# Kernel optimization log

Measured on AMD Instinct MI355X. Metric: run time of the kernel, lower is better.

## Reference

```python
import jax, jax.numpy as jnp
import numpy as np

DUNITS = 1024
ATT_DIM = 1024
EPROJ = 1024
T = 16384
SCALING = 2.0


def setup_inputs() -> dict:
    key = jax.random.key(0)
    ks = jax.random.split(key, 8)
    dec_z = jax.random.normal(ks[0], (1, DUNITS), dtype=jnp.float32)
    att_prev = jnp.zeros((1, T), dtype=jnp.float32)
    pre_compute_enc_h = jax.random.normal(ks[1], (1, T, ATT_DIM), dtype=jnp.float32)
    enc_h = jax.random.normal(ks[2], (1, T, EPROJ), dtype=jnp.float32)
    mask = jnp.zeros((1, T), dtype=jnp.float32)
    # learned params: mlp_dec Linear(dunits->att_dim), gvec Linear(att_dim->1)
    W_dec = jax.random.normal(ks[3], (DUNITS, ATT_DIM), dtype=jnp.float32) / np.sqrt(DUNITS)
    b_dec = jnp.zeros((ATT_DIM,), dtype=jnp.float32)
    w_gvec = jax.random.normal(ks[4], (ATT_DIM,), dtype=jnp.float32) / np.sqrt(ATT_DIM)
    b_gvec = jnp.zeros((), dtype=jnp.float32)
    return {
        "dec_z": dec_z,
        "att_prev": att_prev,
        "pre_compute_enc_h": pre_compute_enc_h,
        "enc_h": enc_h,
        "mask": mask,
        "W_dec": W_dec,
        "b_dec": b_dec,
        "w_gvec": w_gvec,
        "b_gvec": b_gvec,
    }


def reference(dec_z, att_prev, pre_compute_enc_h, enc_h, mask, W_dec, b_dec, w_gvec, b_gvec):
    # dec_z: [1, dunits] -> mlp_dec -> [1, 1, att_dim]
    dec_z_tiled = (dec_z @ W_dec + b_dec)[:, None, :]
    # gvec(tanh(pre + tile)).squeeze(2): [1, T]
    e = jnp.einsum("bta,a->bt", jnp.tanh(pre_compute_enc_h + dec_z_tiled), w_gvec) + b_gvec
    e = e + mask
    w = jax.nn.softmax(SCALING * e, axis=1)  # [1, T]
    c = jnp.einsum("bte,bt->be", enc_h, w)   # [1, eproj]
    return (c, w)
```

## Files before the change

### kernel.cpp

```cpp
#include <hip/hip_runtime.h>
#include <math.h>

#define TT   16384
#define ADIM 1024
#define NCH  512
#define RPW  8
#define NCH2 64

__device__ __forceinline__ float ftanh(float x) {
    float e2 = __expf(2.0f * x);
    return 1.0f - 2.0f * __builtin_amdgcn_rcpf(e2 + 1.0f);
}

__global__ void k1_gemv_part(const float* __restrict__ z, const float* __restrict__ W,
                             float* __restrict__ part) {
    int b = blockIdx.x, tid = threadIdx.x;
    float4 acc = {0.f, 0.f, 0.f, 0.f};
#pragma unroll
    for (int i = 0; i < 4; ++i) {
        int d = b * 4 + i;
        float zv = z[d];
        float4 w4 = reinterpret_cast<const float4*>(W)[(size_t)d * 256 + tid];
        acc.x += zv * w4.x; acc.y += zv * w4.y; acc.z += zv * w4.z; acc.w += zv * w4.w;
    }
    reinterpret_cast<float4*>(part)[(size_t)b * 256 + tid] = acc;
}

__global__ void k2_gemv_red(const float* __restrict__ part, const float* __restrict__ bdec,
                            float* __restrict__ dp) {
    int b = blockIdx.x, tid = threadIdx.x;
    int lane = tid & 63, wv = tid >> 6;
    int rsub = lane >> 2;
    int colg = lane & 3;
    float4 acc = {0.f, 0.f, 0.f, 0.f};
#pragma unroll
    for (int i = 0; i < 4; ++i) {
        int row = i * 64 + wv * 16 + rsub;
        float4 v = reinterpret_cast<const float4*>(part)[(size_t)row * 256 + b * 4 + colg];
        acc.x += v.x; acc.y += v.y; acc.z += v.z; acc.w += v.w;
    }
#pragma unroll
    for (int off = 4; off <= 32; off <<= 1) {
        acc.x += __shfl_xor(acc.x, off, 64);
        acc.y += __shfl_xor(acc.y, off, 64);
        acc.z += __shfl_xor(acc.z, off, 64);
        acc.w += __shfl_xor(acc.w, off, 64);
    }
    __shared__ float4 lds[4][4];
    if (lane < 4) lds[wv][lane] = acc;
    __syncthreads();
    if (tid < 4) {
        float4 t = {0.f, 0.f, 0.f, 0.f};
#pragma unroll
        for (int w = 0; w < 4; ++w) {
            float4 v = lds[w][tid];
            t.x += v.x; t.y += v.y; t.z += v.z; t.w += v.w;
        }
        float4 bd = reinterpret_cast<const float4*>(bdec)[b * 4 + tid];
        t.x += bd.x; t.y += bd.y; t.z += bd.z; t.w += bd.w;
        reinterpret_cast<float4*>(dp)[b * 4 + tid] = t;
    }
}

__global__ void __launch_bounds__(256) k3_fused(
    const float* __restrict__ pre, const float* __restrict__ enc,
    const float* __restrict__ dp, const float* __restrict__ wg,
    const float* __restrict__ bgp, const float* __restrict__ mask,
    float* __restrict__ e_out, float* __restrict__ m_out,
    float* __restrict__ s_out, float* __restrict__ cpart) {
    int b = blockIdx.x, tid = threadIdx.x;
    int lane = tid & 63, wv = tid >> 6;
    float4 d4[4], g4[4];
    const float4* dp4 = reinterpret_cast<const float4*>(dp);
    const float4* wg4 = reinterpret_cast<const float4*>(wg);
#pragma unroll
    for (int j = 0; j < 4; ++j) { d4[j] = dp4[j * 64 + lane]; g4[j] = wg4[j * 64 + lane]; }
    float bgv = bgp[0];
    float m = -3.0e38f, s = 0.f;
    float4 ca[4] = {{0,0,0,0},{0,0,0,0},{0,0,0,0},{0,0,0,0}};
    int t0 = b * (4 * RPW) + wv * RPW;
    for (int i = 0; i < RPW; ++i) {
        int t = t0 + i;
        const float4* pr = reinterpret_cast<const float4*>(pre) + (size_t)t * 256;
        const float4* er = reinterpret_cast<const float4*>(enc) + (size_t)t * 256;
        float4 p[4], ev[4];
#pragma unroll
        for (int j = 0; j < 4; ++j) { p[j] = pr[j * 64 + lane]; ev[j] = er[j * 64 + lane]; }
        float dot = 0.f;
#pragma unroll
        for (int j = 0; j < 4; ++j) {
            dot += ftanh(p[j].x + d4[j].x) * g4[j].x;
            dot += ftanh(p[j].y + d4[j].y) * g4[j].y;
            dot += ftanh(p[j].z + d4[j].z) * g4[j].z;
            dot += ftanh(p[j].w + d4[j].w) * g4[j].w;
        }
#pragma unroll
        for (int off = 32; off; off >>= 1) dot += __shfl_xor(dot, off, 64);
        float et = 2.0f * (dot + bgv + mask[t]);
        if (lane == 0) e_out[t] = et;
        float mn = fmaxf(m, et);
        float sc = __expf(m - mn);
        float pp = __expf(et - mn);
        s = s * sc + pp;
#pragma unroll
        for (int j = 0; j < 4; ++j) {
            ca[j].x = ca[j].x * sc + pp * ev[j].x;
            ca[j].y = ca[j].y * sc + pp * ev[j].y;
            ca[j].z = ca[j].z * sc + pp * ev[j].z;
            ca[j].w = ca[j].w * sc + pp * ev[j].w;
        }
        m = mn;
    }
    __shared__ float lm[4], ls[4];
    __shared__ float4 lc[4][256];
#pragma unroll
    for (int j = 0; j < 4; ++j) lc[wv][j * 64 + lane] = ca[j];
    if (lane == 0) { lm[wv] = m; ls[wv] = s; }
    __syncthreads();
    float Mb = fmaxf(fmaxf(lm[0], lm[1]), fmaxf(lm[2], lm[3]));
    float s0 = __expf(lm[0] - Mb), s1 = __expf(lm[1] - Mb);
    float s2 = __expf(lm[2] - Mb), s3 = __expf(lm[3] - Mb);
    if (tid == 0) {
        m_out[b] = Mb;
        s_out[b] = ls[0] * s0 + ls[1] * s1 + ls[2] * s2 + ls[3] * s3;
    }
    float4 v0 = lc[0][tid], v1 = lc[1][tid], v2 = lc[2][tid], v3 = lc[3][tid];
    float4 o;
    o.x = v0.x * s0 + v1.x * s1 + v2.x * s2 + v3.x * s3;
    o.y = v0.y * s0 + v1.y * s1 + v2.y * s2 + v3.y * s3;
    o.z = v0.z * s0 + v1.z * s1 + v2.z * s2 + v3.z * s3;
    o.w = v0.w * s0 + v1.w * s1 + v2.w * s2 + v3.w * s3;
    reinterpret_cast<float4*>(cpart)[(size_t)b * 256 + tid] = o;
}

__global__ void __launch_bounds__(256) k4_fold(
    const float* __restrict__ m_arr, const float* __restrict__ s_arr,
    const float* __restrict__ cpart, float* __restrict__ cpart2,
    float* __restrict__ msout) {
    int b = blockIdx.x, tid = threadIdx.x;
    int lane = tid & 63, wv = tid >> 6;
    __shared__ float redm[4], reds[4];
    float mloc = fmaxf(m_arr[tid], m_arr[tid + 256]);
#pragma unroll
    for (int off = 32; off; off >>= 1) mloc = fmaxf(mloc, __shfl_xor(mloc, off, 64));
    if (lane == 0) redm[wv] = mloc;
    __syncthreads();
    float M = fmaxf(fmaxf(redm[0], redm[1]), fmaxf(redm[2], redm[3]));
    float4 acc = {0.f, 0.f, 0.f, 0.f};
#pragma unroll
    for (int i = 0; i < 8; ++i) {
        int r = b * 8 + i;
        float sc = __expf(m_arr[r] - M);
        float4 v = reinterpret_cast<const float4*>(cpart)[(size_t)r * 256 + tid];
        acc.x += sc * v.x; acc.y += sc * v.y; acc.z += sc * v.z; acc.w += sc * v.w;
    }
    reinterpret_cast<float4*>(cpart2)[(size_t)b * 256 + tid] = acc;
    if (b == 0) {
        float sl = s_arr[tid] * __expf(m_arr[tid] - M)
                 + s_arr[tid + 256] * __expf(m_arr[tid + 256] - M);
#pragma unroll
        for (int off = 32; off; off >>= 1) sl += __shfl_xor(sl, off, 64);
        if (lane == 0) reds[wv] = sl;
        __syncthreads();
        if (tid == 0) {
            float S = reds[0] + reds[1] + reds[2] + reds[3];
            msout[0] = M;
            msout[1] = 1.0f / S;
        }
    }
}

__global__ void __launch_bounds__(256) k5_final(
    const float* __restrict__ cpart2, const float* __restrict__ e,
    const float* __restrict__ ms, float* __restrict__ c_out,
    float* __restrict__ w_out) {
    int b = blockIdx.x, tid = threadIdx.x;
    float M = ms[0], invS = ms[1];
    if (b < 16) {
        int rs = tid >> 4;
        int cg = tid & 15;
        float4 acc = {0.f, 0.f, 0.f, 0.f};
#pragma unroll
        for (int i = 0; i < 4; ++i) {
            int r = rs * 4 + i;
            float4 v = reinterpret_cast<const float4*>(cpart2)[(size_t)r * 256 + b * 16 + cg];
            acc.x += v.x; acc.y += v.y; acc.z += v.z; acc.w += v.w;
        }
        __shared__ float4 lds[16][16];
        lds[rs][cg] = acc;
        __syncthreads();
        if (tid < 16) {
            float4 t = {0.f, 0.f, 0.f, 0.f};
#pragma unroll
            for (int r = 0; r < 16; ++r) {
                float4 v = lds[r][tid];
                t.x += v.x; t.y += v.y; t.z += v.z; t.w += v.w;
            }
            t.x *= invS; t.y *= invS; t.z *= invS; t.w *= invS;
            reinterpret_cast<float4*>(c_out)[b * 16 + tid] = t;
        }
    } else {
        int base = (b - 16) * 256 + tid;
        float4 ev = reinterpret_cast<const float4*>(e)[base];
        float4 w;
        w.x = __expf(ev.x - M) * invS;
        w.y = __expf(ev.y - M) * invS;
        w.z = __expf(ev.z - M) * invS;
        w.w = __expf(ev.w - M) * invS;
        reinterpret_cast<float4*>(w_out)[base] = w;
    }
}

extern "C" void kernel_launch(void* const* d_in, const int* in_sizes, int n_in,
                              void* d_out, int out_size, void* d_ws, size_t ws_size,
                              hipStream_t stream) {
    const float* dec_z = (const float*)d_in[0];
    const float* pre   = (const float*)d_in[2];
    const float* enc   = (const float*)d_in[3];
    const float* mask  = (const float*)d_in[4];
    const float* W_dec = (const float*)d_in[5];
    const float* b_dec = (const float*)d_in[6];
    const float* wg    = (const float*)d_in[7];
    const float* bg    = (const float*)d_in[8];

    float* out   = (float*)d_out;
    float* c_out = out;
    float* w_out = out + ADIM;

    float* ws = (float*)d_ws;
    float* part   = ws;
    float* dp     = part + 256 * ADIM;
    float* e_sc   = dp + ADIM;
    float* m_arr  = e_sc + TT;
    float* s_arr  = m_arr + NCH;
    float* cpart  = s_arr + NCH;
    float* cpart2 = cpart + (size_t)NCH * ADIM;
    float* ms     = cpart2 + (size_t)NCH2 * ADIM;

    k1_gemv_part<<<256, 256, 0, stream>>>(dec_z, W_dec, part);
    k2_gemv_red<<<64, 256, 0, stream>>>(part, b_dec, dp);
    k3_fused<<<NCH, 256, 0, stream>>>(pre, enc, dp, wg, bg, mask,
                                      e_sc, m_arr, s_arr, cpart);
    k4_fold<<<NCH2, 256, 0, stream>>>(m_arr, s_arr, cpart, cpart2, ms);
    k5_final<<<32, 256, 0, stream>>>(cpart2, e_sc, ms, c_out, w_out);
}
```

Before: 38.01 us.

## Double chunk count and split score and context passes for memory-level parallelism

```diff
diff --git a/kernel.cpp b/kernel.cpp
--- a/kernel.cpp
+++ b/kernel.cpp
@@ -3,8 +3,8 @@
 
 #define TT   16384
 #define ADIM 1024
-#define NCH  512
-#define RPW  8
+#define NCH  1024
+#define RPW  4
 #define NCH2 64
 
 __device__ __forceinline__ float ftanh(float x) {
@@ -76,41 +76,53 @@
 #pragma unroll
     for (int j = 0; j < 4; ++j) { d4[j] = dp4[j * 64 + lane]; g4[j] = wg4[j * 64 + lane]; }
     float bgv = bgp[0];
-    float m = -3.0e38f, s = 0.f;
+    int t0 = b * (4 * RPW) + wv * RPW;
+
+    float et[RPW];
+#pragma unroll
+    for (int i = 0; i < RPW; ++i) {
+        const float4* pr = reinterpret_cast<const float4*>(pre) + (size_t)(t0 + i) * 256;
+        float dot = 0.f;
+#pragma unroll
+        for (int j = 0; j < 4; ++j) {
+            float4 p = pr[j * 64 + lane];
+            dot += ftanh(p.x + d4[j].x) * g4[j].x;
+            dot += ftanh(p.y + d4[j].y) * g4[j].y;
+            dot += ftanh(p.z + d4[j].z) * g4[j].z;
+            dot += ftanh(p.w + d4[j].w) * g4[j].w;
+        }
+        et[i] = dot;
+    }
+#pragma unroll
+    for (int i = 0; i < RPW; ++i) {
+#pragma unroll
+        for (int off = 32; off; off >>= 1) et[i] += __shfl_xor(et[i], off, 64);
+        et[i] = 2.0f * (et[i] + bgv + mask[t0 + i]);
+    }
+    if (lane == 0) {
+#pragma unroll
+        for (int i = 0; i < RPW; ++i) e_out[t0 + i] = et[i];
+    }
+
+    float m = et[0];
+#pragma unroll
+    for (int i = 1; i < RPW; ++i) m = fmaxf(m, et[i]);
+    float p[RPW], s = 0.f;
+#pragma unroll
+    for (int i = 0; i < RPW; ++i) { p[i] = __expf(et[i] - m); s += p[i]; }
+
     float4 ca[4] = {{0,0,0,0},{0,0,0,0},{0,0,0,0},{0,0,0,0}};
-    int t0 = b * (4 * RPW) + wv * RPW;
+#pragma unroll
     for (int i = 0; i < RPW; ++i) {
-        int t = t0 + i;
-        const float4* pr = reinterpret_cast<const float4*>(pre) + (size_t)t * 256;
-        const float4* er = reinterpret_cast<const float4*>(enc) + (size_t)t * 256;
-        float4 p[4], ev[4];
-#pragma unroll
-        for (int j = 0; j < 4; ++j) { p[j] = pr[j * 64 + lane]; ev[j] = er[j * 64 + lane]; }
-        float dot = 0.f;
+        const float4* er = reinterpret_cast<const float4*>(enc) + (size_t)(t0 + i) * 256;
 #pragma unroll
         for (int j = 0; j < 4; ++j) {
-            dot += ftanh(p[j].x + d4[j].x) * g4[j].x;
-            dot += ftanh(p[j].y + d4[j].y) * g4[j].y;
-            dot += ftanh(p[j].z + d4[j].z) * g4[j].z;
-            dot += ftanh(p[j].w + d4[j].w) * g4[j].w;
-        }
-#pragma unroll
-        for (int off = 32; off; off >>= 1) dot += __shfl_xor(dot, off, 64);
-        float et = 2.0f * (dot + bgv + mask[t]);
-        if (lane == 0) e_out[t] = et;
-        float mn = fmaxf(m, et);
-        float sc = __expf(m - mn);
-        float pp = __expf(et - mn);
-        s = s * sc + pp;
-#pragma unroll
-        for (int j = 0; j < 4; ++j) {
-            ca[j].x = ca[j].x * sc + pp * ev[j].x;
-            ca[j].y = ca[j].y * sc + pp * ev[j].y;
-            ca[j].z = ca[j].z * sc + pp * ev[j].z;
-            ca[j].w = ca[j].w * sc + pp * ev[j].w;
-        }
-        m = mn;
-    }
+            float4 v = er[j * 64 + lane];
+            ca[j].x += p[i] * v.x; ca[j].y += p[i] * v.y;
+            ca[j].z += p[i] * v.z; ca[j].w += p[i] * v.w;
+        }
+    }
+
     __shared__ float lm[4], ls[4];
     __shared__ float4 lc[4][256];
 #pragma unroll
@@ -140,7 +152,9 @@
     int b = blockIdx.x, tid = threadIdx.x;
     int lane = tid & 63, wv = tid >> 6;
     __shared__ float redm[4], reds[4];
-    float mloc = fmaxf(m_arr[tid], m_arr[tid + 256]);
+    float mloc = -3.0e38f;
+#pragma unroll
+    for (int i = 0; i < NCH / 256; ++i) mloc = fmaxf(mloc, m_arr[tid + i * 256]);
 #pragma unroll
     for (int off = 32; off; off >>= 1) mloc = fmaxf(mloc, __shfl_xor(mloc, off, 64));
     if (lane == 0) redm[wv] = mloc;
@@ -148,16 +162,18 @@
     float M = fmaxf(fmaxf(redm[0], redm[1]), fmaxf(redm[2], redm[3]));
     float4 acc = {0.f, 0.f, 0.f, 0.f};
 #pragma unroll
-    for (int i = 0; i < 8; ++i) {
-        int r = b * 8 + i;
+    for (int i = 0; i < NCH / NCH2; ++i) {
+        int r = b * (NCH / NCH2) + i;
         float sc = __expf(m_arr[r] - M);
         float4 v = reinterpret_cast<const float4*>(cpart)[(size_t)r * 256 + tid];
         acc.x += sc * v.x; acc.y += sc * v.y; acc.z += sc * v.z; acc.w += sc * v.w;
     }
     reinterpret_cast<float4*>(cpart2)[(size_t)b * 256 + tid] = acc;
     if (b == 0) {
-        float sl = s_arr[tid] * __expf(m_arr[tid] - M)
-                 + s_arr[tid + 256] * __expf(m_arr[tid + 256] - M);
+        float sl = 0.f;
+#pragma unroll
+        for (int i = 0; i < NCH / 256; ++i)
+            sl += s_arr[tid + i * 256] * __expf(m_arr[tid + i * 256] - M);
 #pragma unroll
         for (int off = 32; off; off >>= 1) sl += __shfl_xor(sl, off, 64);
         if (lane == 0) reds[wv] = sl;
```

Result: slower. 41.25 us (+8.5%).
